# Performance work log

Measured on AMD Instinct MI355X. Metric: run time of the kernel, lower is better.

Reference implementation:

```python
import jax, jax.numpy as jnp
import numpy as np

N = 20000      # nodes
E = 640000     # edges
H = 128        # hidden_channels
NB = 16        # num_angle_bins


def setup_inputs() -> dict:
    key = jax.random.key(0)
    ks = jax.random.split(key, 12)
    s = 0.05
    return {
        "x": jax.random.normal(ks[0], (N, H), jnp.float32),
        "pos": jax.random.normal(ks[1], (N, 3), jnp.float32),
        "edge_index": jax.random.randint(ks[2], (2, E), 0, N, dtype=jnp.int32).astype(jnp.int64),
        # edge_mlp: Linear(2H,H) -> silu -> Linear(H,H); weights stored [in,out]
        "W1": jax.random.normal(ks[3], (2 * H, H), jnp.float32) * s,
        "b1": jnp.zeros((H,), jnp.float32),
        "W2": jax.random.normal(ks[4], (H, H), jnp.float32) * s,
        "b2": jnp.zeros((H,), jnp.float32),
        "Wq": jax.random.normal(ks[5], (H, H), jnp.float32) * s,
        "bq": jnp.zeros((H,), jnp.float32),
        "Wk": jax.random.normal(ks[6], (H, H), jnp.float32) * s,
        "bk": jnp.zeros((H,), jnp.float32),
        "Wv": jax.random.normal(ks[7], (H, H), jnp.float32) * s,
        "bv": jnp.zeros((H,), jnp.float32),
    }


def reference(x, pos, edge_index, W1, b1, W2, b2, Wq, bq, Wk, bk, Wv, bv):
    num_nodes, hidden = x.shape
    num_bins = NB
    src = edge_index[0]  # node_i in torch code; PyG suffix _j gathers with this
    dst = edge_index[1]  # node_j in torch code; PyG suffix _i / aggregation index

    # per-edge embedding from endpoint node features  [E, H]
    h = jnp.concatenate([x[src], x[dst]], axis=-1)
    e = jax.nn.silu(h @ W1 + b1) @ W2 + b2

    # unit edge vectors  [E, 3]
    ev = pos[dst] - pos[src]
    ev = ev / (jnp.linalg.norm(ev, axis=1, keepdims=True) + 1e-8)

    q = e @ Wq + bq
    k = e @ Wk + bk
    v = e @ Wv + bv  # computed in torch forward but unused in message (kept for faithfulness)

    # PyG gathers these per-EDGE tensors by NODE indices (node_dim=0) -- replicate exactly
    e_j = e[src]           # [E, H]
    ev_i = ev[dst]         # [E, 3]
    ev_j = ev[src]         # [E, 3]
    q_i = q[dst]           # [E, H]
    k_j = k[src]           # [E, H]

    cos_theta = jnp.clip(jnp.sum(ev_i * ev_j, axis=-1), -1.0, 1.0)  # [E]
    angle_bins = jnp.linspace(-1.0, 1.0, num_bins + 1)
    bin_ids = jnp.clip(jnp.searchsorted(angle_bins, cos_theta, side="left") - 1, 0, num_bins - 1)

    attn_logits = jnp.sum(q_i * k_j, axis=-1) * (1.0 / np.sqrt(hidden))  # [E]

    # grouped softmax over (target_node, angle_bin) pairs, then weighted scatter-add
    group = dst * num_bins + bin_ids                     # [E]
    num_seg = num_nodes * num_bins
    m = jax.ops.segment_max(attn_logits, group, num_segments=num_seg)
    ex = jnp.exp(attn_logits - m[group])
    den = jax.ops.segment_sum(ex, group, num_segments=num_seg)
    attn = ex / (den[group] + 1e-16)                     # [E]

    summed = jax.ops.segment_sum(e_j * attn[:, None], group, num_segments=num_seg)  # [N*B, H]
    out = summed.reshape(num_nodes, num_bins, hidden)
    out = jnp.transpose(out, (0, 2, 1)).reshape(num_nodes, hidden * num_bins)  # [N, H*B]
    return out
```

## Files before the change

### kernel.cpp

```cpp
#include <hip/hip_runtime.h>

#define NN 20000
#define NE 640000
#define HH 128
#define NBIN 16
#define RSQRT_H 0.08838834764831845f

typedef short bf16x8 __attribute__((ext_vector_type(8)));
typedef float f32x4 __attribute__((ext_vector_type(4)));

__device__ __forceinline__ float b2f(unsigned short u) {
    return __uint_as_float(((unsigned)u) << 16);
}
__device__ __forceinline__ unsigned short f2b(float f) {
    unsigned u = __float_as_uint(f);
    unsigned r = (u + 0x7fffu + ((u >> 16) & 1u)) >> 16;
    return (unsigned short)r;
}
__device__ __forceinline__ int clampn(int v) {
    return min(max(v, 0), NN - 1);
}
__device__ __forceinline__ float dotdw(unsigned a, unsigned b) {
    float lo = __uint_as_float(a << 16) * __uint_as_float(b << 16);
    float hi = __uint_as_float(a & 0xffff0000u) * __uint_as_float(b & 0xffff0000u);
    return lo + hi;
}

__global__ __launch_bounds__(256) void k_prep(
    const float* __restrict__ x, ushort* __restrict__ xb,
    const int* __restrict__ ei, const float* __restrict__ pos, float4* __restrict__ ev4,
    const float* __restrict__ W1, const float* __restrict__ W2,
    const float* __restrict__ Wq, const float* __restrict__ Wk,
    ushort* __restrict__ W1T, ushort* __restrict__ W2T, ushort* __restrict__ WqkT,
    unsigned* __restrict__ cnt)
{
    const int bid = blockIdx.x, tid = threadIdx.x;
    if (bid < 2500) {
        int i = bid * 256 + tid;
        float4 v = ((const float4*)x)[i];
        ushort4 o;
        o.x = f2b(v.x); o.y = f2b(v.y); o.z = f2b(v.z); o.w = f2b(v.w);
        ((ushort4*)xb)[i] = o;
    } else if (bid < 2579) {
        int n = (bid - 2500) * 256 + tid;
        if (n < NN) {
            int s = clampn(ei[n]), d = clampn(ei[NE + n]);
            float dx = __fsub_rn(pos[d * 3 + 0], pos[s * 3 + 0]);
            float dy = __fsub_rn(pos[d * 3 + 1], pos[s * 3 + 1]);
            float dz = __fsub_rn(pos[d * 3 + 2], pos[s * 3 + 2]);
            float nsq = __fadd_rn(__fadd_rn(__fmul_rn(dx, dx), __fmul_rn(dy, dy)),
                                  __fmul_rn(dz, dz));
            float den = __fadd_rn(__fsqrt_rn(nsq), 1e-8f);
            float4 o;
            o.x = __fdiv_rn(dx, den); o.y = __fdiv_rn(dy, den);
            o.z = __fdiv_rn(dz, den); o.w = 0.f;
            ev4[n] = o;
        }
    } else if (bid < 2707) {
        int i = (bid - 2579) * 256 + tid;
        if (i < 128 * 256) {
            int c = i >> 8, k = i & 255;
            W1T[i] = f2b(W1[k * 128 + c]);
        }
        if (i < 128 * 128) {
            int c = i >> 7, k = i & 127;
            W2T[i] = f2b(W2[k * 128 + c]);
        }
        if (i < 256 * 128) {
            int c = i >> 7, k = i & 127;
            float v = (c < 128) ? Wq[k * 128 + c] * RSQRT_H : Wk[k * 128 + (c - 128)];
            WqkT[i] = f2b(v);
        }
    } else {
        int i = (bid - 2707) * 256 + tid;
        if (i < NN) cnt[i] = 0u;
    }
}

__global__ __launch_bounds__(256) void k_mlp(
    const int* __restrict__ ei, const ushort* __restrict__ xb,
    const ushort* __restrict__ W1T, const ushort* __restrict__ W2T,
    const ushort* __restrict__ WqkT,
    const float* __restrict__ b1, const float* __restrict__ b2,
    const float* __restrict__ bq, const float* __restrict__ bk,
    ushort* __restrict__ ebuf, ushort* __restrict__ qbuf, ushort* __restrict__ kbuf)
{
    __shared__ ushort A[64][264];
    __shared__ ushort T[4][16][136];
    __shared__ ushort Eb[4][16][136];
    __shared__ int SN[64], DN[64];

    const int tid = threadIdx.x;
    const int wave = tid >> 6, lane = tid & 63;
    const int rw = lane & 15, kq = lane >> 4;
    const int m0 = blockIdx.x * 64;

    if (tid < 64)        SN[tid]      = (m0 + tid < NN)      ? clampn(ei[m0 + tid]) : 0;
    else if (tid < 128)  DN[tid - 64] = (m0 + tid - 64 < NN) ? clampn(ei[NE + m0 + tid - 64]) : 0;
    __syncthreads();

    const unsigned* x32 = (const unsigned*)xb;
    #pragma unroll
    for (int it = 0; it < 32; ++it) {
        int flat = tid + 256 * it;
        int r = flat >> 7, w = flat & 127;
        int node = (w < 64) ? SN[r] : DN[r];
        unsigned val = x32[node * 64 + (w & 63)];
        *(unsigned*)&A[r][2 * w] = val;
    }
    __syncthreads();

    f32x4 acc[8];
    #pragma unroll
    for (int c = 0; c < 8; c++) acc[c] = (f32x4){0.f, 0.f, 0.f, 0.f};
    for (int k0 = 0; k0 < 256; k0 += 32) {
        bf16x8 a = *(const bf16x8*)&A[wave * 16 + rw][k0 + 8 * kq];
        #pragma unroll
        for (int c = 0; c < 8; c++) {
            bf16x8 b = *(const bf16x8*)&W1T[(c * 16 + rw) * 256 + k0 + 8 * kq];
            acc[c] = __builtin_amdgcn_mfma_f32_16x16x32_bf16(a, b, acc[c], 0, 0, 0);
        }
    }
    #pragma unroll
    for (int c = 0; c < 8; c++) {
        float bias = b1[c * 16 + rw];
        #pragma unroll
        for (int r = 0; r < 4; r++) {
            float v = acc[c][r] + bias;
            float s = v / (1.f + __expf(-v));
            T[wave][kq * 4 + r][c * 16 + rw] = f2b(s);
        }
    }
    __syncthreads();

    f32x4 acc2[8];
    #pragma unroll
    for (int c = 0; c < 8; c++) acc2[c] = (f32x4){0.f, 0.f, 0.f, 0.f};
    for (int k0 = 0; k0 < 128; k0 += 32) {
        bf16x8 a = *(const bf16x8*)&T[wave][rw][k0 + 8 * kq];
        #pragma unroll
        for (int c = 0; c < 8; c++) {
            bf16x8 b = *(const bf16x8*)&W2T[(c * 16 + rw) * 128 + k0 + 8 * kq];
            acc2[c] = __builtin_amdgcn_mfma_f32_16x16x32_bf16(a, b, acc2[c], 0, 0, 0);
        }
    }
    #pragma unroll
    for (int c = 0; c < 8; c++) {
        float bias = b2[c * 16 + rw];
        #pragma unroll
        for (int r = 0; r < 4; r++) {
            float v = acc2[c][r] + bias;
            ushort hv = f2b(v);
            Eb[wave][kq * 4 + r][c * 16 + rw] = hv;
            int n = m0 + wave * 16 + kq * 4 + r;
            if (n < NN) ebuf[n * HH + c * 16 + rw] = hv;
        }
    }
    __syncthreads();

    f32x4 acc3[16];
    #pragma unroll
    for (int c = 0; c < 16; c++) acc3[c] = (f32x4){0.f, 0.f, 0.f, 0.f};
    for (int k0 = 0; k0 < 128; k0 += 32) {
        bf16x8 a = *(const bf16x8*)&Eb[wave][rw][k0 + 8 * kq];
        #pragma unroll
        for (int c = 0; c < 16; c++) {
            bf16x8 b = *(const bf16x8*)&WqkT[(c * 16 + rw) * 128 + k0 + 8 * kq];
            acc3[c] = __builtin_amdgcn_mfma_f32_16x16x32_bf16(a, b, acc3[c], 0, 0, 0);
        }
    }
    #pragma unroll
    for (int c = 0; c < 16; c++) {
        int col = c * 16 + rw;
        float bias = (col < 128) ? bq[col] * RSQRT_H : bk[col - 128];
        #pragma unroll
        for (int r = 0; r < 4; r++) {
            float v = acc3[c][r] + bias;
            int n = m0 + wave * 16 + kq * 4 + r;
            if (n < NN) {
                if (col < 128) qbuf[n * HH + col] = f2b(v);
                else           kbuf[n * HH + col - 128] = f2b(v);
            }
        }
    }
}

__global__ void k_hist(const int* __restrict__ ei, unsigned* __restrict__ cnt) {
    int e = blockIdx.x * 256 + threadIdx.x;
    if (e < NE) atomicAdd(&cnt[clampn(ei[NE + e])], 1u);
}

__global__ __launch_bounds__(1024) void k_scan(const unsigned* __restrict__ cnt,
                                               unsigned* __restrict__ starts,
                                               unsigned* __restrict__ cursor) {
    __shared__ unsigned vals[20480];
    __shared__ unsigned wsum[16];
    const int t = threadIdx.x;
    #pragma unroll
    for (int i = 0; i < 20; i++) {
        int idx = i * 1024 + t;
        vals[idx] = (idx < NN) ? cnt[idx] : 0u;
    }
    __syncthreads();
    const int base = t * 20;
    unsigned loc[20];
    unsigned s = 0;
    #pragma unroll
    for (int i = 0; i < 20; i++) { loc[i] = s; s += vals[base + i]; }
    const int lane = t & 63, wv = t >> 6;
    unsigned inc = s;
    #pragma unroll
    for (int o = 1; o < 64; o <<= 1) {
        unsigned y = __shfl_up(inc, o);
        if (lane >= o) inc += y;
    }
    if (lane == 63) wsum[wv] = inc;
    __syncthreads();
    unsigned wbase = 0;
    for (int i = 0; i < wv; i++) wbase += wsum[i];
    unsigned excl = wbase + inc - s;
    #pragma unroll
    for (int i = 0; i < 20; i++) {
        int idx = base + i;
        if (idx < NN) {
            unsigned val = excl + loc[i];
            starts[idx] = val;
            cursor[idx] = val;
        }
    }
    if (t == 1023) starts[NN] = wbase + inc;
}

__global__ __launch_bounds__(256) void k_edge(
    const int* __restrict__ ei, const ushort* __restrict__ qbuf,
    const ushort* __restrict__ kbuf, const float4* __restrict__ ev4,
    unsigned* __restrict__ cursor, uint2* __restrict__ sorted)
{
    int tid = blockIdx.x * 256 + threadIdx.x;
    int e = tid >> 2;
    int r = tid & 3;
    if (e >= NE) return;
    int s = clampn(ei[e]), d = clampn(ei[NE + e]);

    const uint4* q4 = (const uint4*)qbuf;
    const uint4* k4 = (const uint4*)kbuf;
    float p = 0.f;
    #pragma unroll
    for (int i = 0; i < 4; i++) {
        uint4 qw = q4[d * 16 + r * 4 + i];
        uint4 kw = k4[s * 16 + r * 4 + i];
        p += dotdw(qw.x, kw.x) + dotdw(qw.y, kw.y) + dotdw(qw.z, kw.z) + dotdw(qw.w, kw.w);
    }
    p += __shfl_xor(p, 1);
    p += __shfl_xor(p, 2);

    if (r == 0) {
        float4 vi = ev4[d], vj = ev4[s];
        float cosv = __fadd_rn(__fadd_rn(__fmul_rn(vi.x, vj.x), __fmul_rn(vi.y, vj.y)),
                               __fmul_rn(vi.z, vj.z));
        cosv = fminf(fmaxf(cosv, -1.f), 1.f);
        int cntb = 0;
        #pragma unroll
        for (int i = 0; i <= 16; i++) cntb += ((-1.f + 0.125f * (float)i) < cosv) ? 1 : 0;
        int b = min(max(cntb - 1, 0), NBIN - 1);
        unsigned pos = atomicAdd(&cursor[d], 1u);
        sorted[pos] = make_uint2(__float_as_uint(p), (unsigned)((s << 4) | b));
    }
}

__global__ __launch_bounds__(256) void k_node(
    const unsigned* __restrict__ starts, const uint2* __restrict__ sorted,
    const ushort* __restrict__ ebuf, float* __restrict__ out)
{
    const int wave = threadIdx.x >> 6, lane = threadIdx.x & 63;
    const int n = blockIdx.x * 4 + wave;
    __shared__ float den[4][NBIN];

    if (lane < NBIN) den[wave][lane] = 0.f;
    const unsigned s0 = starts[n];
    const int deg = (int)(starts[n + 1] - s0);

    for (int j0 = 0; j0 < deg; j0 += 64) {
        int j = j0 + lane;
        if (j < deg) {
            uint2 m = sorted[s0 + j];
            atomicAdd(&den[wave][m.y & 15u], __expf(__uint_as_float(m.x)));
        }
    }
    if (lane < NBIN) den[wave][lane] = 1.f / (den[wave][lane] + 1e-16f);

    float accx[NBIN], accy[NBIN];
    #pragma unroll
    for (int i = 0; i < NBIN; i++) { accx[i] = 0.f; accy[i] = 0.f; }

    const unsigned* erow = (const unsigned*)ebuf;
    uint2 mN[4];
    #pragma unroll
    for (int i = 0; i < 4; i++)
        mN[i] = (i < deg) ? sorted[s0 + i] : make_uint2(0u, 0u);

#define ACC_CASE(K) case K: accx[K] += w * vx; accy[K] += w * vy; break;
    for (int jb = 0; jb < deg; jb += 4) {
        uint2 m[4];
        #pragma unroll
        for (int i = 0; i < 4; i++) m[i] = mN[i];
        #pragma unroll
        for (int i = 0; i < 4; i++) {
            int j = jb + 4 + i;
            mN[i] = (j < deg) ? sorted[s0 + j] : make_uint2(0u, 0u);
        }
        unsigned rv[4];
        #pragma unroll
        for (int i = 0; i < 4; i++)
            rv[i] = (jb + i < deg) ? erow[(m[i].y >> 4) * 64 + lane] : 0u;
        #pragma unroll
        for (int i = 0; i < 4; i++) {
            if (jb + i < deg) {
                int b = (int)__builtin_amdgcn_readfirstlane(m[i].y & 15u);
                float w = __expf(__uint_as_float(m[i].x)) * den[wave][b];
                float vx = w, vy = w;
                vx = b2f((unsigned short)(rv[i] & 0xffffu));
                vy = b2f((unsigned short)(rv[i] >> 16));
                switch (b) {
                    ACC_CASE(0) ACC_CASE(1) ACC_CASE(2) ACC_CASE(3)
                    ACC_CASE(4) ACC_CASE(5) ACC_CASE(6) ACC_CASE(7)
                    ACC_CASE(8) ACC_CASE(9) ACC_CASE(10) ACC_CASE(11)
                    ACC_CASE(12) ACC_CASE(13) ACC_CASE(14) ACC_CASE(15)
                }
            }
        }
    }
#undef ACC_CASE

    float* op = out + (size_t)n * (HH * NBIN) + 32 * lane;
    #pragma unroll
    for (int j = 0; j < 4; j++) {
        float4 o;
        o.x = accx[4 * j + 0]; o.y = accx[4 * j + 1];
        o.z = accx[4 * j + 2]; o.w = accx[4 * j + 3];
        ((float4*)op)[j] = o;
    }
    #pragma unroll
    for (int j = 0; j < 4; j++) {
        float4 o;
        o.x = accy[4 * j + 0]; o.y = accy[4 * j + 1];
        o.z = accy[4 * j + 2]; o.w = accy[4 * j + 3];
        ((float4*)op)[4 + j] = o;
    }
}

extern "C" void kernel_launch(void* const* d_in, const int* in_sizes, int n_in,
                              void* d_out, int out_size, void* d_ws, size_t ws_size,
                              hipStream_t stream) {
    const float* x        = (const float*)d_in[0];
    const float* pos      = (const float*)d_in[1];
    const int* ei         = (const int*)d_in[2];
    const float* W1       = (const float*)d_in[3];
    const float* b1       = (const float*)d_in[4];
    const float* W2       = (const float*)d_in[5];
    const float* b2       = (const float*)d_in[6];
    const float* Wq       = (const float*)d_in[7];
    const float* bq       = (const float*)d_in[8];
    const float* Wk       = (const float*)d_in[9];
    const float* bk       = (const float*)d_in[10];
    float* out = (float*)d_out;

    char* p = (char*)d_ws;
    auto take = [&](size_t bytes) -> char* {
        char* q = p;
        p += (bytes + 255) & ~(size_t)255;
        return q;
    };
    ushort* xb     = (ushort*)take((size_t)NN * HH * 2);
    ushort* ebuf   = (ushort*)take((size_t)NN * HH * 2);
    ushort* qbuf   = (ushort*)take((size_t)NN * HH * 2);
    ushort* kbuf   = (ushort*)take((size_t)NN * HH * 2);
    float4* ev4    = (float4*)take((size_t)NN * 16);
    ushort* W1T    = (ushort*)take(128 * 256 * 2);
    ushort* W2T    = (ushort*)take(128 * 128 * 2);
    ushort* WqkT   = (ushort*)take(256 * 128 * 2);
    unsigned* cnt  = (unsigned*)take((size_t)NN * 4);
    unsigned* starts = (unsigned*)take((size_t)(NN + 1) * 4);
    unsigned* cursor = (unsigned*)take((size_t)NN * 4);
    uint2* sorted  = (uint2*)take((size_t)NE * 8);
    if ((size_t)(p - (char*)d_ws) > ws_size) return;

    k_prep<<<2786, 256, 0, stream>>>(x, xb, ei, pos, ev4, W1, W2, Wq, Wk,
                                     W1T, W2T, WqkT, cnt);
    k_mlp<<<(NN + 63) / 64, 256, 0, stream>>>(ei, xb, W1T, W2T, WqkT, b1, b2, bq, bk,
                                              ebuf, qbuf, kbuf);
    k_hist<<<(NE + 255) / 256, 256, 0, stream>>>(ei, cnt);
    k_scan<<<1, 1024, 0, stream>>>(cnt, starts, cursor);
    k_edge<<<(NE * 4 + 255) / 256, 256, 0, stream>>>(ei, qbuf, kbuf, ev4, cursor, sorted);
    k_node<<<NN / 4, 256, 0, stream>>>(starts, sorted, ebuf, out);
}
```

Baseline: 430.5 us.

## Fuse softmax denominator into node accumulation pass and precompute exp per edge

The edge kernel now stores exp(logit) instead of the raw logit. The node kernel drops its separate denominator pass with shared-memory atomics. It accumulates per-bin denominators in registers alongside the weighted sums and normalizes with a reciprocal at output time. The gather prefetch depth grows from 4 to 8 edges, which adds register pressure (16 extra accumulators plus larger prefetch buffers) and may lower occupancy. Skipping the max subtraction relies on the logits being small enough that exp does not overflow.

New measurement: 449.8 us. +4.5%, slower.

```diff
diff --git a/kernel.cpp b/kernel.cpp
--- a/kernel.cpp
+++ b/kernel.cpp
@@ -264,7 +264,8 @@
         for (int i = 0; i <= 16; i++) cntb += ((-1.f + 0.125f * (float)i) < cosv) ? 1 : 0;
         int b = min(max(cntb - 1, 0), NBIN - 1);
         unsigned pos = atomicAdd(&cursor[d], 1u);
-        sorted[pos] = make_uint2(__float_as_uint(p), (unsigned)((s << 4) | b));
+        sorted[pos] = make_uint2(__float_as_uint(__expf(p)),
+                                 (unsigned)((s << 4) | b));
     }
 }
 
@@ -274,53 +275,40 @@
 {
     const int wave = threadIdx.x >> 6, lane = threadIdx.x & 63;
     const int n = blockIdx.x * 4 + wave;
-    __shared__ float den[4][NBIN];
-
-    if (lane < NBIN) den[wave][lane] = 0.f;
     const unsigned s0 = starts[n];
     const int deg = (int)(starts[n + 1] - s0);
 
-    for (int j0 = 0; j0 < deg; j0 += 64) {
-        int j = j0 + lane;
-        if (j < deg) {
-            uint2 m = sorted[s0 + j];
-            atomicAdd(&den[wave][m.y & 15u], __expf(__uint_as_float(m.x)));
-        }
-    }
-    if (lane < NBIN) den[wave][lane] = 1.f / (den[wave][lane] + 1e-16f);
-
-    float accx[NBIN], accy[NBIN];
-    #pragma unroll
-    for (int i = 0; i < NBIN; i++) { accx[i] = 0.f; accy[i] = 0.f; }
+    float accx[NBIN], accy[NBIN], accd[NBIN];
+    #pragma unroll
+    for (int i = 0; i < NBIN; i++) { accx[i] = 0.f; accy[i] = 0.f; accd[i] = 0.f; }
 
     const unsigned* erow = (const unsigned*)ebuf;
-    uint2 mN[4];
-    #pragma unroll
-    for (int i = 0; i < 4; i++)
+    uint2 mN[8];
+    #pragma unroll
+    for (int i = 0; i < 8; i++)
         mN[i] = (i < deg) ? sorted[s0 + i] : make_uint2(0u, 0u);
 
-#define ACC_CASE(K) case K: accx[K] += w * vx; accy[K] += w * vy; break;
-    for (int jb = 0; jb < deg; jb += 4) {
-        uint2 m[4];
-        #pragma unroll
-        for (int i = 0; i < 4; i++) m[i] = mN[i];
-        #pragma unroll
-        for (int i = 0; i < 4; i++) {
-            int j = jb + 4 + i;
+#define ACC_CASE(K) case K: accd[K] += ex; accx[K] += ex * vx; accy[K] += ex * vy; break;
+    for (int jb = 0; jb < deg; jb += 8) {
+        uint2 m[8];
+        #pragma unroll
+        for (int i = 0; i < 8; i++) m[i] = mN[i];
+        #pragma unroll
+        for (int i = 0; i < 8; i++) {
+            int j = jb + 8 + i;
             mN[i] = (j < deg) ? sorted[s0 + j] : make_uint2(0u, 0u);
         }
-        unsigned rv[4];
-        #pragma unroll
-        for (int i = 0; i < 4; i++)
+        unsigned rv[8];
+        #pragma unroll
+        for (int i = 0; i < 8; i++)
             rv[i] = (jb + i < deg) ? erow[(m[i].y >> 4) * 64 + lane] : 0u;
         #pragma unroll
-        for (int i = 0; i < 4; i++) {
+        for (int i = 0; i < 8; i++) {
             if (jb + i < deg) {
                 int b = (int)__builtin_amdgcn_readfirstlane(m[i].y & 15u);
-                float w = __expf(__uint_as_float(m[i].x)) * den[wave][b];
-                float vx = w, vy = w;
-                vx = b2f((unsigned short)(rv[i] & 0xffffu));
-                vy = b2f((unsigned short)(rv[i] >> 16));
+                float ex = __uint_as_float(m[i].x);
+                float vx = b2f((unsigned short)(rv[i] & 0xffffu));
+                float vy = b2f((unsigned short)(rv[i] >> 16));
                 switch (b) {
                     ACC_CASE(0) ACC_CASE(1) ACC_CASE(2) ACC_CASE(3)
                     ACC_CASE(4) ACC_CASE(5) ACC_CASE(6) ACC_CASE(7)
@@ -332,19 +320,27 @@
     }
 #undef ACC_CASE
 
+    float inv[NBIN];
+    #pragma unroll
+    for (int i = 0; i < NBIN; i++) inv[i] = __builtin_amdgcn_rcpf(accd[i] + 1e-16f);
+
     float* op = out + (size_t)n * (HH * NBIN) + 32 * lane;
     #pragma unroll
     for (int j = 0; j < 4; j++) {
         float4 o;
-        o.x = accx[4 * j + 0]; o.y = accx[4 * j + 1];
-        o.z = accx[4 * j + 2]; o.w = accx[4 * j + 3];
+        o.x = accx[4 * j + 0] * inv[4 * j + 0];
+        o.y = accx[4 * j + 1] * inv[4 * j + 1];
+        o.z = accx[4 * j + 2] * inv[4 * j + 2];
+        o.w = accx[4 * j + 3] * inv[4 * j + 3];
         ((float4*)op)[j] = o;
     }
     #pragma unroll
     for (int j = 0; j < 4; j++) {
         float4 o;
-        o.x = accy[4 * j + 0]; o.y = accy[4 * j + 1];
-        o.z = accy[4 * j + 2]; o.w = accy[4 * j + 3];
+        o.x = accy[4 * j + 0] * inv[4 * j + 0];
+        o.y = accy[4 * j + 1] * inv[4 * j + 1];
+        o.z = accy[4 * j + 2] * inv[4 * j + 2];
+        o.w = accy[4 * j + 3] * inv[4 * j + 3];
         ((float4*)op)[4 + j] = o;
     }
 }
```
